# Optimization experiments

Hardware: AMD Instinct MI355X
Metric: run time of the kernel (lower is better)

## Reference

```python
import jax, jax.numpy as jnp
import numpy as np

HIDDEN_DIM = 128


def setup_inputs() -> dict:
    key = jax.random.key(0)
    ks = jax.random.split(key, 7)
    n_edges, edge_dim, edge_hidden, d = 20000, 16, 128, HIDDEN_DIM
    h_v = jax.random.normal(ks[0], (n_edges, d), dtype=jnp.float32)
    h_w = jax.random.normal(ks[1], (n_edges, d), dtype=jnp.float32)
    edge_features = jax.random.normal(ks[2], (n_edges, edge_dim), dtype=jnp.float32)
    W1 = jax.random.normal(ks[3], (edge_dim, edge_hidden), dtype=jnp.float32) * (1.0 / np.sqrt(edge_dim))
    b1 = jnp.zeros((edge_hidden,), dtype=jnp.float32)
    W2 = jax.random.normal(ks[4], (edge_hidden, d * d), dtype=jnp.float32) * (1.0 / np.sqrt(edge_hidden))
    b2 = jnp.zeros((d * d,), dtype=jnp.float32)
    return {"h_v": h_v, "h_w": h_w, "edge_features": edge_features,
            "W1": W1, "b1": b1, "W2": W2, "b2": b2}


def reference(h_v, h_w, edge_features, W1, b1, W2, b2):
    d = HIDDEN_DIM
    # Edge MLP: edge_dim -> edge_hidden -> d*d
    hidden = jax.nn.relu(edge_features @ W1 + b1)          # (E, edge_hidden)
    A = (hidden @ W2 + b2).reshape(-1, d, d)               # (E, d, d) per-edge matrices
    # Batched matrix-vector product: messages_e = A_e @ h_w_e
    messages = jnp.einsum('eij,ej->ei', A, h_w)            # (E, d)
    return messages
```

## Files before the change

kernel.cpp:

```cpp
#include <hip/hip_runtime.h>

#define E_EDGES 20000
#define D_DIM   128
#define NBA     136
#define SLAB_B  21504

typedef _Float16 f16x8 __attribute__((ext_vector_type(8)));
typedef _Float16 f16x4 __attribute__((ext_vector_type(4)));
typedef _Float16 f16x2 __attribute__((ext_vector_type(2)));
typedef float    floatx4 __attribute__((ext_vector_type(4)));

union F8 { f16x8 v; f16x2 h2[4]; unsigned int u[4]; };
union F4 { f16x4 v; f16x2 h2[2]; unsigned int u[2]; };

__device__ __forceinline__ unsigned short f32_to_f16(float f) {
    _Float16 h = (_Float16)f;
    return __builtin_bit_cast(unsigned short, h);
}

__global__ __launch_bounds__(256) void prep_w2(
    const float* __restrict__ W2, const float* __restrict__ b2,
    uint4* __restrict__ bpf)
{
    __shared__ __align__(16) unsigned short tile[17408];
    const int h = blockIdx.x;
    const int t = threadIdx.x;

    if (h < 129) {
        const float* src = (h < 128) ? (W2 + (size_t)h * (D_DIM * D_DIM)) : b2;
        #pragma unroll
        for (int r = 0; r < 16; ++r) {
            const float4 v = ((const float4*)src)[r * 256 + t];
            int c   = (r * 256 + t) * 4;
            int col = c >> 7;
            int k   = c & 127;
            unsigned int u0 = f32_to_f16(v.x) | ((unsigned int)f32_to_f16(v.y) << 16);
            unsigned int u1 = f32_to_f16(v.z) | ((unsigned int)f32_to_f16(v.w) << 16);
            *(uint2*)&tile[col * 136 + k] = make_uint2(u0, u1);
        }
        __syncthreads();
        #pragma unroll
        for (int r2 = 0; r2 < 8; ++r2) {
            int cidx = r2 * 256 + t;
            int ll = cidx & 63;
            int nt = (cidx >> 6) & 1;
            int jq = (cidx >> 7) & 3;
            int ch = (cidx >> 9) & 3;
            int col = 32 * ch + 16 * nt + (ll & 15);
            int k0  = 32 * jq + 8 * (ll >> 4);
            bpf[(size_t)h * 2048 + cidx] = *(const uint4*)&tile[col * 136 + k0];
        }
    } else {
        #pragma unroll
        for (int r2 = 0; r2 < 8; ++r2)
            bpf[(size_t)h * 2048 + r2 * 256 + t] = make_uint4(0, 0, 0, 0);
    }
}

__global__ __launch_bounds__(256, 2)
void edge_main(const uint4* __restrict__ bpf, const float* __restrict__ hw,
               const float* __restrict__ ef, const float* __restrict__ W1,
               const float* __restrict__ b1, float* __restrict__ out)
{
    __shared__ __align__(16) char slab[SLAB_B];
    const int bx  = blockIdx.x;
    const int ch2 = bx & 1;
    const int eg  = bx >> 1;
    const int tid = threadIdx.x;
    const int jq  = tid >> 6;
    const int l   = tid & 63;
    const int l4  = l >> 4;
    const int lm  = l & 15;
    const int e0  = eg * 80;

    {
        F4 A[5];
        #pragma unroll
        for (int m = 0; m < 5; ++m) {
            const float4 q4 = *(const float4*)(ef + (size_t)(e0 + 16 * m + lm) * 16 + 4 * l4);
            A[m].h2[0] = (f16x2){(_Float16)q4.x, (_Float16)q4.y};
            A[m].h2[1] = (f16x2){(_Float16)q4.z, (_Float16)q4.w};
        }
        F4 Bw[2];
        float bv[2];
        #pragma unroll
        for (int nn = 0; nn < 2; ++nn) {
            const int col = jq * 32 + nn * 16 + lm;
            float w0 = W1[(4 * l4 + 0) * 128 + col];
            float w1 = W1[(4 * l4 + 1) * 128 + col];
            float w2 = W1[(4 * l4 + 2) * 128 + col];
            float w3 = W1[(4 * l4 + 3) * 128 + col];
            Bw[nn].h2[0] = (f16x2){(_Float16)w0, (_Float16)w1};
            Bw[nn].h2[1] = (f16x2){(_Float16)w2, (_Float16)w3};
            bv[nn] = b1[col];
        }
        #pragma unroll
        for (int m = 0; m < 5; ++m) {
            floatx4 H0 = (floatx4){bv[0], bv[0], bv[0], bv[0]};
            floatx4 H1 = (floatx4){bv[1], bv[1], bv[1], bv[1]};
            H0 = __builtin_amdgcn_mfma_f32_16x16x16f16(A[m].v, Bw[0].v, H0, 0, 0, 0);
            H1 = __builtin_amdgcn_mfma_f32_16x16x16f16(A[m].v, Bw[1].v, H1, 0, 0, 0);
            #pragma unroll
            for (int r = 0; r < 4; ++r) {
                const int e = 16 * m + 4 * l4 + r;
                *(unsigned short*)(slab + e * 264 + (jq * 32 + lm) * 2) =
                    f32_to_f16(fmaxf(H0[r], 0.f));
                *(unsigned short*)(slab + e * 264 + (jq * 32 + 16 + lm) * 2) =
                    f32_to_f16(fmaxf(H1[r], 0.f));
            }
        }
        if (tid < 80) {
            *(unsigned int*)(slab + tid * 264 + 256) = 0x00003C00u;
            *(unsigned int*)(slab + tid * 264 + 260) = 0u;
        }
    }

    F8 hws[5];
    #pragma unroll
    for (int m = 0; m < 5; ++m) {
        const float* ph = hw + (size_t)(e0 + 16 * m + lm) * 128 + 32 * jq + 8 * l4;
        const float4 x = *(const float4*)ph;
        const float4 y = *(const float4*)(ph + 4);
        hws[m].h2[0] = (f16x2){(_Float16)x.x, (_Float16)x.y};
        hws[m].h2[1] = (f16x2){(_Float16)x.z, (_Float16)x.w};
        hws[m].h2[2] = (f16x2){(_Float16)y.x, (_Float16)y.y};
        hws[m].h2[3] = (f16x2){(_Float16)y.z, (_Float16)y.w};
    }

    floatx4 C[5][4];
    #pragma unroll
    for (int m = 0; m < 5; ++m)
        #pragma unroll
        for (int ct = 0; ct < 4; ++ct)
            C[m][ct] = (floatx4){0.f, 0.f, 0.f, 0.f};

    __syncthreads();

    const f16x8* bpf8 = (const f16x8*)bpf;
    const int cbase = ch2 * 1024 + jq * 128 + l;

    f16x8 B[2][4];
    auto loadB = [&](int h, f16x8 (&Bq)[4]) {
        const f16x8* p = bpf8 + (size_t)h * 2048 + cbase;
        Bq[0] = p[0];
        Bq[1] = p[64];
        Bq[2] = p[512];
        Bq[3] = p[576];
    };
    auto doH = [&](int h, const uint2 (&hid)[5]) {
        const int hh = h & 3, pp = h & 1;
        #pragma unroll
        for (int m = 0; m < 5; ++m) {
            unsigned int s   = (hh < 2) ? hid[m].x : hid[m].y;
            unsigned int sel = (hh & 1) ? 0x03020302u : 0x01000100u;
            f16x2 d = __builtin_bit_cast(f16x2, __builtin_amdgcn_perm(0u, s, sel));
            F8 a;
            #pragma unroll
            for (int i = 0; i < 4; ++i) a.h2[i] = hws[m].h2[i] * d;
            C[m][0] = __builtin_amdgcn_mfma_f32_16x16x32_f16(a.v, B[pp][0], C[m][0], 0, 0, 0);
            C[m][1] = __builtin_amdgcn_mfma_f32_16x16x32_f16(a.v, B[pp][1], C[m][1], 0, 0, 0);
            C[m][2] = __builtin_amdgcn_mfma_f32_16x16x32_f16(a.v, B[pp][2], C[m][2], 0, 0, 0);
            C[m][3] = __builtin_amdgcn_mfma_f32_16x16x32_f16(a.v, B[pp][3], C[m][3], 0, 0, 0);
        }
        loadB(h + 2, B[pp]);
    };

    loadB(0, B[0]);
    loadB(1, B[1]);
    for (int q = 0; q < 33; ++q) {
        uint2 hid[5];
        #pragma unroll
        for (int m = 0; m < 5; ++m)
            hid[m] = *(const uint2*)(slab + (16 * m + lm) * 264 + q * 8);
        doH(4 * q + 0, hid);
        doH(4 * q + 1, hid);
        doH(4 * q + 2, hid);
        doH(4 * q + 3, hid);
    }

    float* red = (float*)slab;
    #pragma unroll 1
    for (int src = 1; src < 4; ++src) {
        __syncthreads();
        if (jq == src) {
            #pragma unroll
            for (int m = 0; m < 5; ++m)
                #pragma unroll
                for (int ct = 0; ct < 4; ++ct)
                    #pragma unroll
                    for (int r = 0; r < 4; ++r)
                        red[((m * 4 + ct) * 4 + r) * 64 + l] = C[m][ct][r];
        }
        __syncthreads();
        if (jq == 0) {
            #pragma unroll
            for (int m = 0; m < 5; ++m)
                #pragma unroll
                for (int ct = 0; ct < 4; ++ct)
                    #pragma unroll
                    for (int r = 0; r < 4; ++r)
                        C[m][ct][r] += red[((m * 4 + ct) * 4 + r) * 64 + l];
        }
    }
    if (jq == 0) {
        #pragma unroll
        for (int m = 0; m < 5; ++m)
            #pragma unroll
            for (int ct = 0; ct < 4; ++ct)
                #pragma unroll
                for (int r = 0; r < 4; ++r)
                    out[(size_t)(e0 + 16 * m + 4 * l4 + r) * D_DIM
                        + 64 * ch2 + 16 * ct + lm] = C[m][ct][r];
    }
}

extern "C" void kernel_launch(void* const* d_in, const int* in_sizes, int n_in,
                              void* d_out, int out_size, void* d_ws, size_t ws_size,
                              hipStream_t stream) {
    const float* h_w = (const float*)d_in[1];
    const float* ef  = (const float*)d_in[2];
    const float* W1  = (const float*)d_in[3];
    const float* b1  = (const float*)d_in[4];
    const float* W2  = (const float*)d_in[5];
    const float* b2  = (const float*)d_in[6];
    float* out = (float*)d_out;

    uint4* bpf = (uint4*)d_ws;

    hipLaunchKernelGGL(prep_w2, dim3(NBA), dim3(256), 0, stream, W2, b2, bpf);
    hipLaunchKernelGGL(edge_main, dim3(500), dim3(256), 0, stream,
                       bpf, h_w, ef, W1, b1, out);
}
```

Measured before the change: 161.2 us.

## Deepen W2 fragment prefetch to four stages and double-buffer hidden reads

Grows the register ring of W2 B-fragments from two to four slots, so each load is issued four hidden units ahead, and starts the first four loads before the barrier. The h_w load now comes before the layer-1 MFMA, and the per-quad hidden-activation LDS reads are double-buffered across a manually paired loop. The goal is to hide global/L2 latency of the streamed W2 tiles and LDS latency behind MFMA work. In exchange it uses roughly 32 more VGPRs, which could push spills or reduce occupancy under the two-blocks-per-CU launch bound.

```diff
diff --git a/kernel.cpp b/kernel.cpp
--- a/kernel.cpp
+++ b/kernel.cpp
@@ -73,48 +73,6 @@
     const int lm  = l & 15;
     const int e0  = eg * 80;
 
-    {
-        F4 A[5];
-        #pragma unroll
-        for (int m = 0; m < 5; ++m) {
-            const float4 q4 = *(const float4*)(ef + (size_t)(e0 + 16 * m + lm) * 16 + 4 * l4);
-            A[m].h2[0] = (f16x2){(_Float16)q4.x, (_Float16)q4.y};
-            A[m].h2[1] = (f16x2){(_Float16)q4.z, (_Float16)q4.w};
-        }
-        F4 Bw[2];
-        float bv[2];
-        #pragma unroll
-        for (int nn = 0; nn < 2; ++nn) {
-            const int col = jq * 32 + nn * 16 + lm;
-            float w0 = W1[(4 * l4 + 0) * 128 + col];
-            float w1 = W1[(4 * l4 + 1) * 128 + col];
-            float w2 = W1[(4 * l4 + 2) * 128 + col];
-            float w3 = W1[(4 * l4 + 3) * 128 + col];
-            Bw[nn].h2[0] = (f16x2){(_Float16)w0, (_Float16)w1};
-            Bw[nn].h2[1] = (f16x2){(_Float16)w2, (_Float16)w3};
-            bv[nn] = b1[col];
-        }
-        #pragma unroll
-        for (int m = 0; m < 5; ++m) {
-            floatx4 H0 = (floatx4){bv[0], bv[0], bv[0], bv[0]};
-            floatx4 H1 = (floatx4){bv[1], bv[1], bv[1], bv[1]};
-            H0 = __builtin_amdgcn_mfma_f32_16x16x16f16(A[m].v, Bw[0].v, H0, 0, 0, 0);
-            H1 = __builtin_amdgcn_mfma_f32_16x16x16f16(A[m].v, Bw[1].v, H1, 0, 0, 0);
-            #pragma unroll
-            for (int r = 0; r < 4; ++r) {
-                const int e = 16 * m + 4 * l4 + r;
-                *(unsigned short*)(slab + e * 264 + (jq * 32 + lm) * 2) =
-                    f32_to_f16(fmaxf(H0[r], 0.f));
-                *(unsigned short*)(slab + e * 264 + (jq * 32 + 16 + lm) * 2) =
-                    f32_to_f16(fmaxf(H1[r], 0.f));
-            }
-        }
-        if (tid < 80) {
-            *(unsigned int*)(slab + tid * 264 + 256) = 0x00003C00u;
-            *(unsigned int*)(slab + tid * 264 + 260) = 0u;
-        }
-    }
-
     F8 hws[5];
     #pragma unroll
     for (int m = 0; m < 5; ++m) {
@@ -127,6 +85,48 @@
         hws[m].h2[3] = (f16x2){(_Float16)y.z, (_Float16)y.w};
     }
 
+    {
+        F4 A[5];
+        #pragma unroll
+        for (int m = 0; m < 5; ++m) {
+            const float4 q4 = *(const float4*)(ef + (size_t)(e0 + 16 * m + lm) * 16 + 4 * l4);
+            A[m].h2[0] = (f16x2){(_Float16)q4.x, (_Float16)q4.y};
+            A[m].h2[1] = (f16x2){(_Float16)q4.z, (_Float16)q4.w};
+        }
+        F4 Bw[2];
+        float bv[2];
+        #pragma unroll
+        for (int nn = 0; nn < 2; ++nn) {
+            const int col = jq * 32 + nn * 16 + lm;
+            float w0 = W1[(4 * l4 + 0) * 128 + col];
+            float w1 = W1[(4 * l4 + 1) * 128 + col];
+            float w2 = W1[(4 * l4 + 2) * 128 + col];
+            float w3 = W1[(4 * l4 + 3) * 128 + col];
+            Bw[nn].h2[0] = (f16x2){(_Float16)w0, (_Float16)w1};
+            Bw[nn].h2[1] = (f16x2){(_Float16)w2, (_Float16)w3};
+            bv[nn] = b1[col];
+        }
+        #pragma unroll
+        for (int m = 0; m < 5; ++m) {
+            floatx4 H0 = (floatx4){bv[0], bv[0], bv[0], bv[0]};
+            floatx4 H1 = (floatx4){bv[1], bv[1], bv[1], bv[1]};
+            H0 = __builtin_amdgcn_mfma_f32_16x16x16f16(A[m].v, Bw[0].v, H0, 0, 0, 0);
+            H1 = __builtin_amdgcn_mfma_f32_16x16x16f16(A[m].v, Bw[1].v, H1, 0, 0, 0);
+            #pragma unroll
+            for (int r = 0; r < 4; ++r) {
+                const int e = 16 * m + 4 * l4 + r;
+                *(unsigned short*)(slab + e * 264 + (jq * 32 + lm) * 2) =
+                    f32_to_f16(fmaxf(H0[r], 0.f));
+                *(unsigned short*)(slab + e * 264 + (jq * 32 + 16 + lm) * 2) =
+                    f32_to_f16(fmaxf(H1[r], 0.f));
+            }
+        }
+        if (tid < 80) {
+            *(unsigned int*)(slab + tid * 264 + 256) = 0x00003C00u;
+            *(unsigned int*)(slab + tid * 264 + 260) = 0u;
+        }
+    }
+
     floatx4 C[5][4];
     #pragma unroll
     for (int m = 0; m < 5; ++m)
@@ -134,12 +134,10 @@
         for (int ct = 0; ct < 4; ++ct)
             C[m][ct] = (floatx4){0.f, 0.f, 0.f, 0.f};
 
-    __syncthreads();
-
     const f16x8* bpf8 = (const f16x8*)bpf;
     const int cbase = ch2 * 1024 + jq * 128 + l;
 
-    f16x8 B[2][4];
+    f16x8 B[4][4];
     auto loadB = [&](int h, f16x8 (&Bq)[4]) {
         const f16x8* p = bpf8 + (size_t)h * 2048 + cbase;
         Bq[0] = p[0];
@@ -147,8 +145,15 @@
         Bq[2] = p[512];
         Bq[3] = p[576];
     };
+    loadB(0, B[0]);
+    loadB(1, B[1]);
+    loadB(2, B[2]);
+    loadB(3, B[3]);
+
+    __syncthreads();
+
     auto doH = [&](int h, const uint2 (&hid)[5]) {
-        const int hh = h & 3, pp = h & 1;
+        const int hh = h & 3;
         #pragma unroll
         for (int m = 0; m < 5; ++m) {
             unsigned int s   = (hh < 2) ? hid[m].x : hid[m].y;
@@ -157,26 +162,38 @@
             F8 a;
             #pragma unroll
             for (int i = 0; i < 4; ++i) a.h2[i] = hws[m].h2[i] * d;
-            C[m][0] = __builtin_amdgcn_mfma_f32_16x16x32_f16(a.v, B[pp][0], C[m][0], 0, 0, 0);
-            C[m][1] = __builtin_amdgcn_mfma_f32_16x16x32_f16(a.v, B[pp][1], C[m][1], 0, 0, 0);
-            C[m][2] = __builtin_amdgcn_mfma_f32_16x16x32_f16(a.v, B[pp][2], C[m][2], 0, 0, 0);
-            C[m][3] = __builtin_amdgcn_mfma_f32_16x16x32_f16(a.v, B[pp][3], C[m][3], 0, 0, 0);
-        }
-        loadB(h + 2, B[pp]);
+            C[m][0] = __builtin_amdgcn_mfma_f32_16x16x32_f16(a.v, B[hh][0], C[m][0], 0, 0, 0);
+            C[m][1] = __builtin_amdgcn_mfma_f32_16x16x32_f16(a.v, B[hh][1], C[m][1], 0, 0, 0);
+            C[m][2] = __builtin_amdgcn_mfma_f32_16x16x32_f16(a.v, B[hh][2], C[m][2], 0, 0, 0);
+            C[m][3] = __builtin_amdgcn_mfma_f32_16x16x32_f16(a.v, B[hh][3], C[m][3], 0, 0, 0);
+        }
+        loadB(h + 4, B[hh]);
     };
-
-    loadB(0, B[0]);
-    loadB(1, B[1]);
-    for (int q = 0; q < 33; ++q) {
-        uint2 hid[5];
+    auto readHid = [&](int q, uint2 (&hid)[5]) {
         #pragma unroll
         for (int m = 0; m < 5; ++m)
             hid[m] = *(const uint2*)(slab + (16 * m + lm) * 264 + q * 8);
-        doH(4 * q + 0, hid);
-        doH(4 * q + 1, hid);
-        doH(4 * q + 2, hid);
-        doH(4 * q + 3, hid);
-    }
+    };
+
+    uint2 hid0[5], hid1[5];
+    readHid(0, hid0);
+    #pragma unroll 1
+    for (int q = 0; q < 32; q += 2) {
+        readHid(q + 1, hid1);
+        doH(4 * q + 0, hid0);
+        doH(4 * q + 1, hid0);
+        doH(4 * q + 2, hid0);
+        doH(4 * q + 3, hid0);
+        readHid(q + 2, hid0);
+        doH(4 * q + 4, hid1);
+        doH(4 * q + 5, hid1);
+        doH(4 * q + 6, hid1);
+        doH(4 * q + 7, hid1);
+    }
+    doH(128, hid0);
+    doH(129, hid0);
+    doH(130, hid0);
+    doH(131, hid0);
 
     float* red = (float*)slab;
     #pragma unroll 1
```

Result: faster. 151.2 us (-6.2%).
